# Optimization experiments

Measured on AMD Instinct MI355X. Metric: run time of the kernel, lower is better.

## Reference

```python
import jax, jax.numpy as jnp
import numpy as np

BASE_BITS = 17            # tokens < 2**17; pack n-gram tuple into one int64
NGRAM_SIZES = (2, 3)      # sorted(ngram_to_size.keys())
TABLE_SIZE = 100000       # ngram_to_size[n]
ID_OFFSET = 4             # vocab ids start at 4 in the original
B, S, VOCAB = 256, 16384, 50000


def _encode_windows(x, n):
    """x: [B,S] int tokens -> [B,S] int64, each entry encodes the left-padded
    n-gram window (t[i-n+1],...,t[i]) exactly like the original tuple key."""
    b, s = x.shape
    padded = jnp.pad(x.astype(jnp.int64), ((0, 0), (n - 1, 0)))  # constant 0 pad, as in np.pad
    enc = jnp.zeros((b, s), dtype=jnp.int64)
    for i in range(n):  # tiny fixed loop over window size
        enc = (enc << BASE_BITS) | padded[:, i:i + s]
    return enc


def _lookup(enc, keys, vals):
    """dict.get(tuple(window), 0) as sorted-array hash-probe: searchsorted + verify."""
    flat = enc.reshape(-1)
    idx = jnp.clip(jnp.searchsorted(keys, flat), 0, keys.shape[0] - 1)
    hit = keys[idx] == flat
    return jnp.where(hit, vals[idx], 0).reshape(enc.shape)


def setup_inputs() -> dict:
    rng = np.random.default_rng(0)
    x = rng.integers(0, VOCAB, size=(B, S), dtype=np.int64)
    inp = {"x": jnp.asarray(x)}
    xj = jnp.asarray(x)
    for n in NGRAM_SIZES:
        # Build vocab tables from n-grams actually present so lookups hit,
        # mirroring update_from_batch() having seen similar data.
        enc = np.asarray(_encode_windows(xj, n)).reshape(-1)
        uniq = np.unique(enc)
        take = min(TABLE_SIZE, uniq.size)
        keys = np.sort(rng.choice(uniq, size=take, replace=False)).astype(np.int64)
        vals = (rng.permutation(take) + ID_OFFSET).astype(np.int64)  # ids 4..take+3
        inp[f"keys{n}"] = jnp.asarray(keys)
        inp[f"vals{n}"] = jnp.asarray(vals)
    return inp


def reference(x, keys2, vals2, keys3, vals3):
    tables = {2: (keys2, vals2), 3: (keys3, vals3)}
    # encode_token_ngrams + stack_ngrams -> [len(NGRAM_SIZES), B, S]
    outs = [_lookup(_encode_windows(x, n), *tables[n]) for n in NGRAM_SIZES]
    return jnp.stack(outs, axis=0)
```

## Files before the change

kernel.cpp:

```cpp
#include <hip/hip_runtime.h>

#define BASE_BITS 17
#define BUCKET_LOG 16
#define NBUCKETS (1u << BUCKET_LOG)
#define NSLOTS (NBUCKETS * 4u)
#define SLOT_MASK (NSLOTS - 1u)
#define BUCKET_MASK (NBUCKETS - 1u)
#define EMPTY 0xFFFFFFFFu

#define BF_LOG 17
#define BF_WORDS (1u << (BF_LOG - 5))

typedef int  iv4 __attribute__((ext_vector_type(4)));
typedef unsigned uv4 __attribute__((ext_vector_type(4)));

__device__ __forceinline__ unsigned bucket_of(unsigned k) {
    return (k * 2654435761u) >> (32 - BUCKET_LOG);
}
__device__ __forceinline__ unsigned bloom_of(unsigned k) {
    return (k * 0x85EBCA77u) >> (32 - BF_LOG);
}

__device__ __forceinline__ int match4(uv4 q, unsigned e, unsigned b) {
    int slot = -1;
    slot = (q.w == e) ? (int)(b * 4u + 3u) : slot;
    slot = (q.z == e) ? (int)(b * 4u + 2u) : slot;
    slot = (q.y == e) ? (int)(b * 4u + 1u) : slot;
    slot = (q.x == e) ? (int)(b * 4u + 0u) : slot;
    if (slot >= 0) return slot;
    unsigned mx = max(max(q.x, q.y), max(q.z, q.w));
    return (mx == EMPTY) ? -2 : -1;
}

__global__ void detect_dtype_kernel(const unsigned* __restrict__ xw,
                                    int* __restrict__ flags) {
    __shared__ int nz;
    if (threadIdx.x == 0) nz = 0;
    __syncthreads();
    if (xw[2 * threadIdx.x + 1] != 0u) atomicOr(&nz, 1);
    __syncthreads();
    if (threadIdx.x == 0) { flags[0] = nz ? 0 : ~0; flags[1] = 0; }
}

__global__ void build_hash_kernel(const int* __restrict__ keys2,
                                  const int* __restrict__ vals2, int n2,
                                  const int* __restrict__ keys3,
                                  const int* __restrict__ vals3, int n3,
                                  const unsigned* __restrict__ xw,
                                  unsigned* __restrict__ K2, int* __restrict__ V2,
                                  unsigned* __restrict__ K3, int* __restrict__ V3,
                                  unsigned* __restrict__ BF2,
                                  unsigned* __restrict__ BF3,
                                  int* __restrict__ flags) {
    int i = blockIdx.x * blockDim.x + threadIdx.x;
    if (i < 256 && xw[2 * i + 1] != 0u) atomicAnd(&flags[0], 0);

    const int* keys; const int* vals; unsigned* K; int* V; unsigned* BF; int idx;
    if (i < n2)           { keys = keys2; vals = vals2; K = K2; V = V2; BF = BF2; idx = i; }
    else if (i < n2 + n3) { keys = keys3; vals = vals3; K = K3; V = V3; BF = BF3; idx = i - n2; }
    else return;
    unsigned k = (unsigned)keys[idx];
    if (k == EMPTY) { atomicAnd(&flags[1], 0); return; }
    unsigned h = bloom_of(k);
    atomicAnd(&BF[h >> 5], ~(1u << (h & 31u)));
    unsigned slot = bucket_of(k) * 4u;
    for (;;) {
        unsigned prev = atomicCAS(&K[slot], EMPTY, k);
        if (prev == EMPTY) { V[slot] = vals[idx]; break; }
        slot = (slot + 1u) & SLOT_MASK;
    }
}

template <typename K>
__device__ __forceinline__ int lower_bound(const K* __restrict__ keys, int n, K key) {
    int lo = 0, hi = n;
    while (lo < hi) {
        int mid = (lo + hi) >> 1;
        if (keys[mid] < key) lo = mid + 1; else hi = mid;
    }
    return lo;
}

template <typename K>
__device__ __forceinline__ K bprobe(const K* __restrict__ keys,
                                    const K* __restrict__ vals, int n, K key) {
    int idx = lower_bound(keys, n, key);
    if (idx >= n) idx = n - 1;
    return (keys[idx] == key) ? vals[idx] : (K)0;
}

__global__ __launch_bounds__(256) void ngram_hash_kernel(
    const void* __restrict__ xv,
    const unsigned* __restrict__ K2, const int* __restrict__ V2,
    const unsigned* __restrict__ K3, const int* __restrict__ V3,
    const unsigned* __restrict__ gBF2, const unsigned* __restrict__ gBF3,
    const void* __restrict__ k2v, const void* __restrict__ v2v,
    const void* __restrict__ k3v, const void* __restrict__ v3v,
    void* __restrict__ outv,
    int n2, int n3, int S, int total, const int* __restrict__ flags)
{
    int tid0 = blockIdx.x * blockDim.x + threadIdx.x;
    int nth = gridDim.x * blockDim.x;
    int ntask = (total + 3) / 4;
    int f0 = flags[0], f1 = flags[1];

    if (f0 != 0) {
        const long long* x = (const long long*)xv;
        long long* out = (long long*)outv;
        for (int task = tid0; task < ntask; task += nth) {
            int base = task * 4;
            for (int i = 0; i < 4 && base + i < total; ++i) {
                int g = base + i;
                int s = g & (S - 1);
                long long t2 = x[g];
                long long t1 = (s >= 1) ? x[g - 1] : 0ll;
                long long t0 = (s >= 2) ? x[g - 2] : 0ll;
                long long e2 = (t1 << BASE_BITS) | t2;
                long long e3 = (((t0 << BASE_BITS) | t1) << BASE_BITS) | t2;
                out[g]         = bprobe((const long long*)k2v, (const long long*)v2v, n2, e2);
                out[total + g] = bprobe((const long long*)k3v, (const long long*)v3v, n3, e3);
            }
        }
        return;
    }
    if (f1 == 0) {
        const int* x = (const int*)xv;
        int* out = (int*)outv;
        for (int task = tid0; task < ntask; task += nth) {
            int base = task * 4;
            for (int i = 0; i < 4 && base + i < total; ++i) {
                int g = base + i;
                int s = g & (S - 1);
                unsigned t2 = (unsigned)x[g];
                unsigned t1 = (s >= 1) ? (unsigned)x[g - 1] : 0u;
                unsigned t0 = (s >= 2) ? (unsigned)x[g - 2] : 0u;
                int e2 = (int)((t1 << BASE_BITS) | t2);
                int e3 = (int)((((t0 << BASE_BITS) | t1) << BASE_BITS) | t2);
                out[g]         = bprobe((const int*)k2v, (const int*)v2v, n2, e2);
                out[total + g] = bprobe((const int*)k3v, (const int*)v3v, n3, e3);
            }
        }
        return;
    }

    __shared__ unsigned bf2[BF_WORDS];
    __shared__ unsigned bf3[BF_WORDS];
    {
        const uv4* s2 = (const uv4*)gBF2;
        const uv4* s3 = (const uv4*)gBF3;
        uv4* d2 = (uv4*)bf2;
        uv4* d3 = (uv4*)bf3;
        for (unsigned w = threadIdx.x; w < BF_WORDS / 4; w += 256) {
            d2[w] = s2[w];
            d3[w] = s3[w];
        }
    }
    __syncthreads();

    const int* x = (const int*)xv;
    const uv4* KB2 = (const uv4*)K2;
    const uv4* KB3 = (const uv4*)K3;

    for (int task = tid0; task < ntask; task += nth) {
        int base = task * 4;
        if (base + 3 >= total) {
            int* out = (int*)outv;
            for (int i = 0; i < 4 && base + i < total; ++i) {
                int g = base + i;
                int s = g & (S - 1);
                unsigned t2 = (unsigned)x[g];
                unsigned t1 = (s >= 1) ? (unsigned)x[g - 1] : 0u;
                unsigned t0 = (s >= 2) ? (unsigned)x[g - 2] : 0u;
                unsigned e2 = (t1 << BASE_BITS) | t2;
                unsigned e3 = (((t0 << BASE_BITS) | t1) << BASE_BITS) | t2;
                unsigned bb2 = bucket_of(e2), bb3 = bucket_of(e3);
                int s2v = match4(KB2[bb2], e2, bb2);
                while (s2v == -1) { bb2 = (bb2 + 1u) & BUCKET_MASK; s2v = match4(KB2[bb2], e2, bb2); }
                int s3v = match4(KB3[bb3], e3, bb3);
                while (s3v == -1) { bb3 = (bb3 + 1u) & BUCKET_MASK; s3v = match4(KB3[bb3], e3, bb3); }
                out[g]         = (s2v >= 0) ? V2[s2v] : 0;
                out[total + g] = (s3v >= 0) ? V3[s3v] : 0;
            }
            continue;
        }

        iv4 xq = __builtin_nontemporal_load(&((const iv4*)x)[task]);
        int sb = base & (S - 1);
        unsigned t[6];
        t[0] = (sb != 0) ? (unsigned)x[base - 2] : 0u;
        t[1] = (sb != 0) ? (unsigned)x[base - 1] : 0u;
        t[2] = (unsigned)xq.x; t[3] = (unsigned)xq.y;
        t[4] = (unsigned)xq.z; t[5] = (unsigned)xq.w;

        unsigned e[8], b[8];
        bool maybe[8];
        #pragma unroll
        for (int i = 0; i < 4; ++i) {
            unsigned t0 = t[i], t1 = t[i + 1], t2 = t[i + 2];
            e[i]     = (t1 << BASE_BITS) | t2;
            e[i + 4] = (((t0 << BASE_BITS) | t1) << BASE_BITS) | t2;
        }
        #pragma unroll
        for (int i = 0; i < 8; ++i) {
            b[i] = bucket_of(e[i]);
            unsigned h = bloom_of(e[i]);
            unsigned w = (i < 4 ? bf2 : bf3)[h >> 5];
            maybe[i] = ((w >> (h & 31u)) & 1u) == 0u;
        }

        const uv4* a0 = maybe[0] ? KB2 + b[0] : KB2;
        const uv4* a1 = maybe[1] ? KB2 + b[1] : KB2;
        const uv4* a2 = maybe[2] ? KB2 + b[2] : KB2;
        const uv4* a3 = maybe[3] ? KB2 + b[3] : KB2;
        const uv4* a4 = maybe[4] ? KB3 + b[4] : KB3;
        const uv4* a5 = maybe[5] ? KB3 + b[5] : KB3;
        const uv4* a6 = maybe[6] ? KB3 + b[6] : KB3;
        const uv4* a7 = maybe[7] ? KB3 + b[7] : KB3;
        uv4 q0, q1, q2, q3, q4, q5, q6, q7;
        asm volatile(
            "global_load_dwordx4 %0, %8, off\n\t"
            "global_load_dwordx4 %1, %9, off\n\t"
            "global_load_dwordx4 %2, %10, off\n\t"
            "global_load_dwordx4 %3, %11, off\n\t"
            "global_load_dwordx4 %4, %12, off\n\t"
            "global_load_dwordx4 %5, %13, off\n\t"
            "global_load_dwordx4 %6, %14, off\n\t"
            "global_load_dwordx4 %7, %15, off\n\t"
            "s_waitcnt vmcnt(0)"
            : "=&v"(q0), "=&v"(q1), "=&v"(q2), "=&v"(q3),
              "=&v"(q4), "=&v"(q5), "=&v"(q6), "=&v"(q7)
            : "v"(a0), "v"(a1), "v"(a2), "v"(a3),
              "v"(a4), "v"(a5), "v"(a6), "v"(a7)
            : "memory");

        int st[8];
        st[0] = maybe[0] ? match4(q0, e[0], b[0]) : -2;
        st[1] = maybe[1] ? match4(q1, e[1], b[1]) : -2;
        st[2] = maybe[2] ? match4(q2, e[2], b[2]) : -2;
        st[3] = maybe[3] ? match4(q3, e[3], b[3]) : -2;
        st[4] = maybe[4] ? match4(q4, e[4], b[4]) : -2;
        st[5] = maybe[5] ? match4(q5, e[5], b[5]) : -2;
        st[6] = maybe[6] ? match4(q6, e[6], b[6]) : -2;
        st[7] = maybe[7] ? match4(q7, e[7], b[7]) : -2;

        bool cont = false;
        #pragma unroll
        for (int i = 0; i < 8; ++i) cont |= (st[i] == -1);
        while (__any(cont)) {
            #pragma unroll
            for (int i = 0; i < 8; ++i) {
                if (st[i] == -1) {
                    b[i] = (b[i] + 1u) & BUCKET_MASK;
                    uv4 nq = (i < 4 ? KB2 : KB3)[b[i]];
                    st[i] = match4(nq, e[i], b[i]);
                }
            }
            cont = false;
            #pragma unroll
            for (int i = 0; i < 8; ++i) cont |= (st[i] == -1);
        }

        int r[8];
        #pragma unroll
        for (int i = 0; i < 8; ++i)
            r[i] = (st[i] >= 0) ? (i < 4 ? V2 : V3)[st[i]] : 0;

        iv4 o2 = { r[0], r[1], r[2], r[3] };
        iv4 o3 = { r[4], r[5], r[6], r[7] };
        __builtin_nontemporal_store(o2, &((iv4*)outv)[task]);
        __builtin_nontemporal_store(o3, &((iv4*)outv)[total / 4 + task]);
    }
}

extern "C" void kernel_launch(void* const* d_in, const int* in_sizes, int n_in,
                              void* d_out, int out_size, void* d_ws, size_t ws_size,
                              hipStream_t stream) {
    const void* x  = d_in[0];
    const void* k2 = d_in[1];
    const void* v2 = d_in[2];
    const void* k3 = d_in[3];
    const void* v3 = d_in[4];
    int n2 = in_sizes[1];
    int n3 = in_sizes[3];
    int total = in_sizes[0];
    int S = 16384;

    int* flags = (int*)d_ws;
    size_t key_bytes = (size_t)NSLOTS * 4;
    size_t bf_bytes  = (size_t)BF_WORDS * 4;
    size_t need = 256 + 2 * key_bytes + 2 * bf_bytes + 2 * key_bytes;

    int ncu = 256;
    (void)hipDeviceGetAttribute(&ncu, hipDeviceAttributeMultiprocessorCount, 0);
    int grid = 5 * ncu;
    if (grid < 64) grid = 64;

    if (ws_size >= need) {
        unsigned* K2  = (unsigned*)((char*)d_ws + 256);
        unsigned* K3  = K2 + NSLOTS;
        unsigned* BF2 = K3 + NSLOTS;
        unsigned* BF3 = BF2 + BF_WORDS;
        int* V2 = (int*)(BF3 + BF_WORDS);
        int* V3 = V2 + NSLOTS;

        (void)hipMemsetAsync(d_ws, 0xFF, 256 + 2 * key_bytes + 2 * bf_bytes, stream);

        build_hash_kernel<<<(n2 + n3 + 255) / 256, 256, 0, stream>>>(
            (const int*)k2, (const int*)v2, n2,
            (const int*)k3, (const int*)v3, n3,
            (const unsigned*)x, K2, V2, K3, V3, BF2, BF3, flags);

        ngram_hash_kernel<<<grid, 256, 0, stream>>>(
            x, K2, V2, K3, V3, BF2, BF3, k2, v2, k3, v3,
            d_out, n2, n3, S, total, flags);
    } else {
        detect_dtype_kernel<<<1, 256, 0, stream>>>((const unsigned*)x, flags);
        ngram_hash_kernel<<<grid, 256, 0, stream>>>(
            x, nullptr, nullptr, nullptr, nullptr, nullptr, nullptr,
            k2, v2, k3, v3, d_out, n2, n3, S, total, flags);
    }
}
```

Measured before the change: 104.9 us.

## Share neighbor tokens via wave shuffle and predicate bucket loads instead of asm

Gets the two preceding tokens from the neighboring lane with __shfl_up, so only lane 0 of each wavefront issues the two extra global loads. Replaces the inline-asm batch of eight unconditional bucket loads (with a dummy address for bloom-rejected keys) with predicated C++ loads that fall back to an all-EMPTY vector. Value loads are also predicated. This cuts redundant memory traffic for bloom-filtered misses, but lets the compiler schedule the loads and waits, which may reduce memory-level parallelism. It also relies on match4 returning -2 for an all-EMPTY bucket.

```diff
diff --git a/kernel.cpp b/kernel.cpp
--- a/kernel.cpp
+++ b/kernel.cpp
@@ -186,9 +186,16 @@
 
         iv4 xq = __builtin_nontemporal_load(&((const iv4*)x)[task]);
         int sb = base & (S - 1);
+
+        unsigned upz = (unsigned)__shfl_up(xq.z, 1);
+        unsigned upw = (unsigned)__shfl_up(xq.w, 1);
+        if ((threadIdx.x & 63) == 0 && sb != 0) {
+            upz = (unsigned)x[base - 2];
+            upw = (unsigned)x[base - 1];
+        }
         unsigned t[6];
-        t[0] = (sb != 0) ? (unsigned)x[base - 2] : 0u;
-        t[1] = (sb != 0) ? (unsigned)x[base - 1] : 0u;
+        t[0] = (sb != 0) ? upz : 0u;
+        t[1] = (sb != 0) ? upw : 0u;
         t[2] = (unsigned)xq.x; t[3] = (unsigned)xq.y;
         t[4] = (unsigned)xq.z; t[5] = (unsigned)xq.w;
 
@@ -208,40 +215,22 @@
             maybe[i] = ((w >> (h & 31u)) & 1u) == 0u;
         }
 
-        const uv4* a0 = maybe[0] ? KB2 + b[0] : KB2;
-        const uv4* a1 = maybe[1] ? KB2 + b[1] : KB2;
-        const uv4* a2 = maybe[2] ? KB2 + b[2] : KB2;
-        const uv4* a3 = maybe[3] ? KB2 + b[3] : KB2;
-        const uv4* a4 = maybe[4] ? KB3 + b[4] : KB3;
-        const uv4* a5 = maybe[5] ? KB3 + b[5] : KB3;
-        const uv4* a6 = maybe[6] ? KB3 + b[6] : KB3;
-        const uv4* a7 = maybe[7] ? KB3 + b[7] : KB3;
-        uv4 q0, q1, q2, q3, q4, q5, q6, q7;
-        asm volatile(
-            "global_load_dwordx4 %0, %8, off\n\t"
-            "global_load_dwordx4 %1, %9, off\n\t"
-            "global_load_dwordx4 %2, %10, off\n\t"
-            "global_load_dwordx4 %3, %11, off\n\t"
-            "global_load_dwordx4 %4, %12, off\n\t"
-            "global_load_dwordx4 %5, %13, off\n\t"
-            "global_load_dwordx4 %6, %14, off\n\t"
-            "global_load_dwordx4 %7, %15, off\n\t"
-            "s_waitcnt vmcnt(0)"
-            : "=&v"(q0), "=&v"(q1), "=&v"(q2), "=&v"(q3),
-              "=&v"(q4), "=&v"(q5), "=&v"(q6), "=&v"(q7)
-            : "v"(a0), "v"(a1), "v"(a2), "v"(a3),
-              "v"(a4), "v"(a5), "v"(a6), "v"(a7)
-            : "memory");
+        uv4 q[8];
+        uv4 none = { EMPTY, EMPTY, EMPTY, EMPTY };
+        #pragma unroll
+        for (int i = 0; i < 8; ++i) q[i] = none;
+        if (maybe[0]) q[0] = KB2[b[0]];
+        if (maybe[1]) q[1] = KB2[b[1]];
+        if (maybe[2]) q[2] = KB2[b[2]];
+        if (maybe[3]) q[3] = KB2[b[3]];
+        if (maybe[4]) q[4] = KB3[b[4]];
+        if (maybe[5]) q[5] = KB3[b[5]];
+        if (maybe[6]) q[6] = KB3[b[6]];
+        if (maybe[7]) q[7] = KB3[b[7]];
 
         int st[8];
-        st[0] = maybe[0] ? match4(q0, e[0], b[0]) : -2;
-        st[1] = maybe[1] ? match4(q1, e[1], b[1]) : -2;
-        st[2] = maybe[2] ? match4(q2, e[2], b[2]) : -2;
-        st[3] = maybe[3] ? match4(q3, e[3], b[3]) : -2;
-        st[4] = maybe[4] ? match4(q4, e[4], b[4]) : -2;
-        st[5] = maybe[5] ? match4(q5, e[5], b[5]) : -2;
-        st[6] = maybe[6] ? match4(q6, e[6], b[6]) : -2;
-        st[7] = maybe[7] ? match4(q7, e[7], b[7]) : -2;
+        #pragma unroll
+        for (int i = 0; i < 8; ++i) st[i] = match4(q[i], e[i], b[i]);
 
         bool cont = false;
         #pragma unroll
@@ -262,8 +251,15 @@
 
         int r[8];
         #pragma unroll
-        for (int i = 0; i < 8; ++i)
-            r[i] = (st[i] >= 0) ? (i < 4 ? V2 : V3)[st[i]] : 0;
+        for (int i = 0; i < 8; ++i) r[i] = 0;
+        if (st[0] >= 0) r[0] = V2[st[0]];
+        if (st[1] >= 0) r[1] = V2[st[1]];
+        if (st[2] >= 0) r[2] = V2[st[2]];
+        if (st[3] >= 0) r[3] = V2[st[3]];
+        if (st[4] >= 0) r[4] = V3[st[4]];
+        if (st[5] >= 0) r[5] = V3[st[5]];
+        if (st[6] >= 0) r[6] = V3[st[6]];
+        if (st[7] >= 0) r[7] = V3[st[7]];
 
         iv4 o2 = { r[0], r[1], r[2], r[3] };
         iv4 o3 = { r[4], r[5], r[6], r[7] };
```

Measured after the change: 105.0 us. No clear change (+0.1%).
